# Performance work log

Hardware: AMD Instinct MI355X
Metric: run time of the kernel (lower is better)

Reference implementation:

```python
import jax, jax.numpy as jnp
import numpy as np

LATENT = 64
OUT = 128
H1 = 32
H2 = 32
N = 65536


def setup_inputs() -> dict:
    key = jax.random.key(0)
    ks = jax.random.split(key, 8)
    # kaiming-normal-ish std for relu: sqrt(2/fan_in)
    z = jax.random.normal(ks[0], (N, LATENT), dtype=jnp.float32)
    Wp = jax.random.normal(ks[1], (OUT, LATENT), dtype=jnp.float32)  # LinearP weight, init.normal_
    # per-feature tiny MLP params, stacked over the OUT features
    W1 = jax.random.normal(ks[2], (OUT, H1), dtype=jnp.float32) * jnp.sqrt(2.0 / 1.0)   # Linear(1,H1).weight -> [H1,1] per feature
    b1 = jnp.zeros((OUT, H1), dtype=jnp.float32)
    W2 = jax.random.normal(ks[3], (OUT, H2, H1), dtype=jnp.float32) * jnp.sqrt(2.0 / H1)  # Linear(H1,H2).weight
    b2 = jnp.zeros((OUT, H2), dtype=jnp.float32)
    W3 = jax.random.normal(ks[4], (OUT, H2), dtype=jnp.float32) * jnp.sqrt(2.0 / H2)   # Linear(H2,1).weight -> [1,H2] per feature
    b3 = jnp.zeros((OUT,), dtype=jnp.float32)
    return {"z": z, "Wp": Wp, "W1": W1, "b1": b1, "W2": W2, "b2": b2, "W3": W3, "b3": b3}


def reference(z, Wp, W1, b1, W2, b2, W3, b3):
    # LinearP: y = z @ |Wp|^T, no bias
    y = jnp.einsum('nl,dl->nd', z, jnp.abs(Wp))          # [N, OUT]
    # Per-feature tiny MLPs, fully batched over the feature dim d.
    # layer 1: input size 1 -> H1
    h = jax.nn.relu(y[..., None] * W1 + b1)              # [N, OUT, H1]
    # layer 2: H1 -> H2
    h = jax.nn.relu(jnp.einsum('ndh,dkh->ndk', h, W2) + b2)  # [N, OUT, H2]
    # output layer: H2 -> 1, then abs over the concatenated components
    x = jnp.einsum('ndh,dh->nd', h, W3) + b3             # [N, OUT]
    return jnp.abs(x)
```

## Files before the change

kernel.cpp:

```cpp
#include <hip/hip_runtime.h>
#include <hip/hip_bf16.h>

typedef unsigned int uint32;
typedef __attribute__((ext_vector_type(8))) short    bf16x8;
typedef __attribute__((ext_vector_type(4))) float    f32x4;
typedef __attribute__((ext_vector_type(8))) _Float16 f16x8;
typedef __attribute__((ext_vector_type(2))) _Float16 f16x2;

#define MFMA_BF(A, B, C) __builtin_amdgcn_mfma_f32_16x16x32_bf16(A, B, C, 0, 0, 0)
#define MFMA_F16(A, B, C) __builtin_amdgcn_mfma_f32_16x16x32_f16(A, B, C, 0, 0, 0)

union FragU { uint32 u[4]; bf16x8 v; };
union H8    { f16x2 h[4]; f16x8 v; };

__device__ __forceinline__ void split8(f32x4 a, f32x4 b, bf16x8& hi, bf16x8& lo) {
    float e[8] = {a[0], a[1], a[2], a[3], b[0], b[1], b[2], b[3]};
    FragU H, L;
    #pragma unroll
    for (int q = 0; q < 4; ++q) {
        uint32 u0 = __float_as_uint(e[2*q]);
        uint32 u1 = __float_as_uint(e[2*q + 1]);
        uint32 h0 = u0 & 0xFFFF0000u;
        uint32 h1 = u1 & 0xFFFF0000u;
        float l0 = e[2*q]     - __uint_as_float(h0);
        float l1 = e[2*q + 1] - __uint_as_float(h1);
        H.u[q] = (h0 >> 16) | h1;
        L.u[q] = (__float_as_uint(l0) >> 16) | (__float_as_uint(l1) & 0xFFFF0000u);
    }
    hi = H.v; lo = L.v;
}

__global__ __launch_bounds__(256) void split_weights(
    const float* __restrict__ Wp, const float* __restrict__ W2,
    const float* __restrict__ W1, const float* __restrict__ b1,
    __hip_bfloat16* __restrict__ wp_hi, __hip_bfloat16* __restrict__ wp_lo,
    _Float16* __restrict__ w2h, f16x2* __restrict__ w1p, f16x2* __restrict__ b1p)
{
    const int i = blockIdx.x * 256 + threadIdx.x;
    if (i < 128 * 64) {
        float x = fabsf(Wp[i]);
        __hip_bfloat16 h = __float2bfloat16(x);
        wp_hi[i] = h;
        wp_lo[i] = __float2bfloat16(x - __bfloat162float(h));
    }
    if (i < 128 * 1024) {
        w2h[i] = (_Float16)W2[i];
    }
    if (i < 128 * 16) {
        const int d = i >> 4, q = i & 15;
        f16x2 a, b;
        a[0] = (_Float16)W1[d*32 + 2*q];  a[1] = (_Float16)W1[d*32 + 2*q + 1];
        b[0] = (_Float16)b1[d*32 + 2*q];  b[1] = (_Float16)b1[d*32 + 2*q + 1];
        w1p[i] = a;  b1p[i] = b;
    }
}

__global__ __launch_bounds__(64, 4) void decoder_mfma(
    const float* __restrict__ z,
    const __hip_bfloat16* __restrict__ wp_hi, const __hip_bfloat16* __restrict__ wp_lo,
    const _Float16* __restrict__ w2h,
    const f16x2* __restrict__ w1p, const f16x2* __restrict__ b1p,
    const float* __restrict__ b2,
    const float* __restrict__ W3, const float* __restrict__ b3,
    float* __restrict__ out)
{
    __shared__ float Y[64][33];

    const int lane = threadIdx.x;
    const int l15  = lane & 15;
    const int lg   = lane >> 4;
    const int g    = blockIdx.x & 3;
    const int n0   = (blockIdx.x >> 2) * 64;

    bf16x8 wh[2][2], wl[2][2];
    #pragma unroll
    for (int dt = 0; dt < 2; ++dt) {
        const int d = g*32 + dt*16 + l15;
        #pragma unroll
        for (int kt = 0; kt < 2; ++kt) {
            const int off = d*64 + kt*32 + lg*8;
            wh[dt][kt] = *(const bf16x8*)(wp_hi + off);
            wl[dt][kt] = *(const bf16x8*)(wp_lo + off);
        }
    }
    #pragma unroll
    for (int nt = 0; nt < 4; ++nt) {
        bf16x8 zh[2], zl[2];
        #pragma unroll
        for (int kt = 0; kt < 2; ++kt) {
            const float* p = z + (size_t)(n0 + nt*16 + l15)*64 + kt*32 + lg*8;
            split8(*(const f32x4*)p, *(const f32x4*)(p + 4), zh[kt], zl[kt]);
        }
        #pragma unroll
        for (int dt = 0; dt < 2; ++dt) {
            f32x4 acc = {0.f, 0.f, 0.f, 0.f};
            #pragma unroll
            for (int kt = 0; kt < 2; ++kt) {
                acc = MFMA_BF(zh[kt], wh[dt][kt], acc);
                acc = MFMA_BF(zl[kt], wh[dt][kt], acc);
                acc = MFMA_BF(zh[kt], wl[dt][kt], acc);
            }
            #pragma unroll
            for (int r = 0; r < 4; ++r)
                Y[nt*16 + lg*4 + r][dt*16 + l15] = acc[r];
        }
    }
    __syncthreads();

    const f16x2 zero2 = {(_Float16)0.f, (_Float16)0.f};
    #pragma unroll 4
    for (int j = 0; j < 32; ++j) {
        const int d = g*32 + j;
        const f16x8 ah0 = *(const f16x8*)(w2h + d*1024 + l15*32 + lg*8);
        const f16x8 ah1 = *(const f16x8*)(w2h + d*1024 + (16 + l15)*32 + lg*8);
        H8 w1u, b1u;
        w1u.v = *(const f16x8*)(w1p + d*16 + lg*4);
        b1u.v = *(const f16x8*)(b1p + d*16 + lg*4);
        const f32x4 b2a = *(const f32x4*)(b2 + d*32 + lg*4);
        const f32x4 b2b = *(const f32x4*)(b2 + d*32 + 16 + lg*4);
        const f32x4 w3a = *(const f32x4*)(W3 + d*32 + lg*4);
        const f32x4 w3b = *(const f32x4*)(W3 + d*32 + 16 + lg*4);
        const float b3v = b3[d];

        float yv[4];
        #pragma unroll
        for (int ct = 0; ct < 4; ++ct) yv[ct] = Y[ct*16 + l15][j];

        f16x8 pk[4];
        #pragma unroll
        for (int ct = 0; ct < 4; ++ct) {
            const _Float16 yh = (_Float16)yv[ct];
            const f16x2 y2 = {yh, yh};
            H8 u;
            #pragma unroll
            for (int q = 0; q < 4; ++q)
                u.h[q] = __builtin_elementwise_max(
                             __builtin_elementwise_fma(y2, w1u.h[q], b1u.h[q]),
                             zero2);
            pk[ct] = u.v;
        }

        f32x4 A0[4], A1[4];
        #pragma unroll
        for (int ct = 0; ct < 4; ++ct) { A0[ct] = b2a; A1[ct] = b2b; }
        #pragma unroll
        for (int ct = 0; ct < 4; ++ct) {
            A0[ct] = MFMA_F16(ah0, pk[ct], A0[ct]);
            A1[ct] = MFMA_F16(ah1, pk[ct], A1[ct]);
        }

        #pragma unroll
        for (int ct = 0; ct < 4; ++ct) {
            float s = fmaxf(A0[ct][0], 0.f) * w3a[0];
            s = fmaf(fmaxf(A0[ct][1], 0.f), w3a[1], s);
            s = fmaf(fmaxf(A0[ct][2], 0.f), w3a[2], s);
            s = fmaf(fmaxf(A0[ct][3], 0.f), w3a[3], s);
            s = fmaf(fmaxf(A1[ct][0], 0.f), w3b[0], s);
            s = fmaf(fmaxf(A1[ct][1], 0.f), w3b[1], s);
            s = fmaf(fmaxf(A1[ct][2], 0.f), w3b[2], s);
            s = fmaf(fmaxf(A1[ct][3], 0.f), w3b[3], s);
            s += __shfl_xor(s, 16);
            s += __shfl_xor(s, 32);
            const float x = fabsf(s + b3v);
            if (lane < 16) Y[ct*16 + lane][j] = x;
        }
    }
    __syncthreads();

    const int cg = lane & 7;
    #pragma unroll
    for (int it = 0; it < 8; ++it) {
        const int n = it*8 + (lane >> 3);
        f32x4 v;
        #pragma unroll
        for (int c = 0; c < 4; ++c) v[c] = Y[n][cg*4 + c];
        *(f32x4*)(out + (size_t)(n0 + n)*128 + g*32 + cg*4) = v;
    }
}

extern "C" void kernel_launch(void* const* d_in, const int* in_sizes, int n_in,
                              void* d_out, int out_size, void* d_ws, size_t ws_size,
                              hipStream_t stream) {
    const float* z  = (const float*)d_in[0];
    const float* Wp = (const float*)d_in[1];
    const float* W1 = (const float*)d_in[2];
    const float* b1 = (const float*)d_in[3];
    const float* W2 = (const float*)d_in[4];
    const float* b2 = (const float*)d_in[5];
    const float* W3 = (const float*)d_in[6];
    const float* b3 = (const float*)d_in[7];
    float* out = (float*)d_out;

    __hip_bfloat16* wp_hi = (__hip_bfloat16*)d_ws;
    __hip_bfloat16* wp_lo = wp_hi + 128 * 64;
    _Float16*       w2h   = (_Float16*)(wp_lo + 128 * 64);
    f16x2*          w1p   = (f16x2*)(w2h + 128 * 1024);
    f16x2*          b1p   = w1p + 128 * 16;

    hipLaunchKernelGGL(split_weights, dim3(512), dim3(256), 0, stream,
                       Wp, W2, W1, b1, wp_hi, wp_lo, w2h, w1p, b1p);
    hipLaunchKernelGGL(decoder_mfma, dim3(4096), dim3(64), 0, stream,
                       z, wp_hi, wp_lo, w2h, w1p, b1p, b2, W3, b3, out);
}
```

Baseline: 65.68 us.

## Merge feature-group blocks into 4-wave blocks with per-wave fp16 LDS tiles

Replaces four single-wave blocks per 64-row tile with one 256-thread block where each wave handles one 32-feature group using its own LDS slice, removing block barriers. The intermediate Y tile and the final outputs are stored in LDS as fp16 instead of fp32, halving LDS footprint. This aims to improve occupancy and reduce scheduling overhead, but rounds the final output to fp16 before writing, which can reduce accuracy.

```diff
diff --git a/kernel.cpp b/kernel.cpp
--- a/kernel.cpp
+++ b/kernel.cpp
@@ -5,6 +5,7 @@
 typedef __attribute__((ext_vector_type(8))) short    bf16x8;
 typedef __attribute__((ext_vector_type(4))) float    f32x4;
 typedef __attribute__((ext_vector_type(8))) _Float16 f16x8;
+typedef __attribute__((ext_vector_type(4))) _Float16 f16x4;
 typedef __attribute__((ext_vector_type(2))) _Float16 f16x2;
 
 #define MFMA_BF(A, B, C) __builtin_amdgcn_mfma_f32_16x16x32_bf16(A, B, C, 0, 0, 0)
@@ -55,7 +56,7 @@
     }
 }
 
-__global__ __launch_bounds__(64, 4) void decoder_mfma(
+__global__ __launch_bounds__(256, 8) void decoder_mfma(
     const float* __restrict__ z,
     const __hip_bfloat16* __restrict__ wp_hi, const __hip_bfloat16* __restrict__ wp_lo,
     const _Float16* __restrict__ w2h,
@@ -64,18 +65,19 @@
     const float* __restrict__ W3, const float* __restrict__ b3,
     float* __restrict__ out)
 {
-    __shared__ float Y[64][33];
-
-    const int lane = threadIdx.x;
+    __shared__ __align__(16) _Float16 Y[4][64][36];
+
+    const int t    = threadIdx.x;
+    const int lane = t & 63;
+    const int wv   = __builtin_amdgcn_readfirstlane(t >> 6);
     const int l15  = lane & 15;
     const int lg   = lane >> 4;
-    const int g    = blockIdx.x & 3;
-    const int n0   = (blockIdx.x >> 2) * 64;
+    const int n0   = blockIdx.x * 64;
 
     bf16x8 wh[2][2], wl[2][2];
     #pragma unroll
     for (int dt = 0; dt < 2; ++dt) {
-        const int d = g*32 + dt*16 + l15;
+        const int d = wv*32 + dt*16 + l15;
         #pragma unroll
         for (int kt = 0; kt < 2; ++kt) {
             const int off = d*64 + kt*32 + lg*8;
@@ -102,15 +104,14 @@
             }
             #pragma unroll
             for (int r = 0; r < 4; ++r)
-                Y[nt*16 + lg*4 + r][dt*16 + l15] = acc[r];
-        }
-    }
-    __syncthreads();
+                Y[wv][nt*16 + lg*4 + r][dt*16 + l15] = (_Float16)acc[r];
+        }
+    }
 
     const f16x2 zero2 = {(_Float16)0.f, (_Float16)0.f};
     #pragma unroll 4
     for (int j = 0; j < 32; ++j) {
-        const int d = g*32 + j;
+        const int d = wv*32 + j;
         const f16x8 ah0 = *(const f16x8*)(w2h + d*1024 + l15*32 + lg*8);
         const f16x8 ah1 = *(const f16x8*)(w2h + d*1024 + (16 + l15)*32 + lg*8);
         H8 w1u, b1u;
@@ -122,15 +123,14 @@
         const f32x4 w3b = *(const f32x4*)(W3 + d*32 + 16 + lg*4);
         const float b3v = b3[d];
 
-        float yv[4];
-        #pragma unroll
-        for (int ct = 0; ct < 4; ++ct) yv[ct] = Y[ct*16 + l15][j];
+        _Float16 yv[4];
+        #pragma unroll
+        for (int ct = 0; ct < 4; ++ct) yv[ct] = Y[wv][ct*16 + l15][j];
 
         f16x8 pk[4];
         #pragma unroll
         for (int ct = 0; ct < 4; ++ct) {
-            const _Float16 yh = (_Float16)yv[ct];
-            const f16x2 y2 = {yh, yh};
+            const f16x2 y2 = {yv[ct], yv[ct]};
             H8 u;
             #pragma unroll
             for (int q = 0; q < 4; ++q)
@@ -162,19 +162,19 @@
             s += __shfl_xor(s, 16);
             s += __shfl_xor(s, 32);
             const float x = fabsf(s + b3v);
-            if (lane < 16) Y[ct*16 + lane][j] = x;
-        }
-    }
-    __syncthreads();
+            if (lane < 16) Y[wv][ct*16 + lane][j] = (_Float16)x;
+        }
+    }
 
     const int cg = lane & 7;
     #pragma unroll
     for (int it = 0; it < 8; ++it) {
         const int n = it*8 + (lane >> 3);
+        const f16x4 h = *(const f16x4*)&Y[wv][n][cg*4];
         f32x4 v;
         #pragma unroll
-        for (int c = 0; c < 4; ++c) v[c] = Y[n][cg*4 + c];
-        *(f32x4*)(out + (size_t)(n0 + n)*128 + g*32 + cg*4) = v;
+        for (int c = 0; c < 4; ++c) v[c] = (float)h[c];
+        *(f32x4*)(out + (size_t)(n0 + n)*128 + wv*32 + cg*4) = v;
     }
 }
 
@@ -199,6 +199,6 @@
 
     hipLaunchKernelGGL(split_weights, dim3(512), dim3(256), 0, stream,
                        Wp, W2, W1, b1, wp_hi, wp_lo, w2h, w1p, b1p);
-    hipLaunchKernelGGL(decoder_mfma, dim3(4096), dim3(64), 0, stream,
+    hipLaunchKernelGGL(decoder_mfma, dim3(1024), dim3(256), 0, stream,
                        z, wp_hi, wp_lo, w2h, w1p, b1p, b2, W3, b3, out);
 }
```

Result: slower. 88.02 us (+34.0%).
